# Performance work log

Measured on AMD Instinct MI355X. Metric: run time of the kernel, lower is better.

Reference implementation:

```python
import jax, jax.numpy as jnp
import numpy as np

NUM_HEADS = 24
HEAD_DIM = 128
EPS = 1e-6


def setup_inputs() -> dict:
    key = jax.random.key(0)
    k0, k1, k2 = jax.random.split(key, 3)
    B, S, dim = 2, 2048, 3072
    hidden_states = jax.random.normal(k0, (B, S, dim), dtype=jnp.float32)
    image_rotary_emb = jax.random.normal(k1, (1, 1, S, HEAD_DIM // 2, 2, 2), dtype=jnp.float32)
    w_qkv = jax.random.normal(k2, (dim, 3 * dim), dtype=jnp.float32) * 0.02
    b_qkv = jnp.zeros((3 * dim,), dtype=jnp.float32)
    norm_q_w = jnp.ones((HEAD_DIM,), dtype=jnp.float32)
    norm_k_w = jnp.ones((HEAD_DIM,), dtype=jnp.float32)
    return {
        "hidden_states": hidden_states,
        "image_rotary_emb": image_rotary_emb,
        "w_qkv": w_qkv,
        "b_qkv": b_qkv,
        "norm_q_w": norm_q_w,
        "norm_k_w": norm_k_w,
    }


def _rmsnorm(x, w):
    # RMSNorm over last dim (head_dim)
    var = jnp.mean(x * x, axis=-1, keepdims=True)
    return x * jax.lax.rsqrt(var + EPS) * w


def _apply_rope(x, freqs_cis):
    # x: [B,H,S,D]; freqs_cis: [1,1,S,D//2,2,2]
    B, H, S, D = x.shape
    x_ = x.reshape(B, H, S, D // 2, 1, 2)
    out = freqs_cis[..., 0] * x_[..., 0] + freqs_cis[..., 1] * x_[..., 1]  # [B,H,S,D//2,2]
    return out.reshape(B, H, S, D)


def reference(hidden_states, image_rotary_emb, w_qkv, b_qkv, norm_q_w, norm_k_w):
    B, S, _ = hidden_states.shape
    H, D = NUM_HEADS, HEAD_DIM
    qkv = hidden_states @ w_qkv + b_qkv                 # [B,S,3*H*D]
    qkv = qkv.reshape(B, S, 3, H, D)
    q = jnp.moveaxis(qkv[:, :, 0], 1, 2)                # [B,H,S,D]
    k = jnp.moveaxis(qkv[:, :, 1], 1, 2)
    v = jnp.moveaxis(qkv[:, :, 2], 1, 2)
    q = _rmsnorm(q, norm_q_w)
    k = _rmsnorm(k, norm_k_w)
    q = _apply_rope(q, image_rotary_emb)
    k = _apply_rope(k, image_rotary_emb)
    scale = 1.0 / jnp.sqrt(jnp.asarray(D, dtype=q.dtype))
    scores = jnp.einsum("bhqd,bhkd->bhqk", q, k) * scale
    attn = jax.nn.softmax(scores, axis=-1)
    out = jnp.einsum("bhqk,bhkd->bhqd", attn, v)        # [B,H,S,D]
    out = jnp.moveaxis(out, 1, 2).reshape(B, S, H * D)  # [B,S,H*D]
    return out
```

## Files before the change

### kernel.cpp

```cpp
#include <hip/hip_runtime.h>


#define SS 2048
#define BB 2
#define HH 24
#define DD 128
#define KDIM 3072
#define N3 9216
#define MM 4096

typedef float f32x4 __attribute__((ext_vector_type(4)));
typedef __bf16 bf16x8 __attribute__((ext_vector_type(8)));

__device__ __forceinline__ unsigned short f2b(float f) {
  union { float f; unsigned int u; } v; v.f = f;
  unsigned int u = v.u;
  u += 0x7FFFu + ((u >> 16) & 1u);
  return (unsigned short)(u >> 16);
}
__device__ __forceinline__ float b2f(unsigned short b) {
  union { unsigned int u; float f; } v; v.u = ((unsigned int)b) << 16; return v.f;
}
__device__ __forceinline__ f32x4 mfma16(bf16x8 a, bf16x8 b, f32x4 c) {
  return __builtin_amdgcn_mfma_f32_16x16x32_bf16(a, b, c, 0, 0, 0);
}
typedef __attribute__((address_space(1))) void gas_void;
typedef __attribute__((address_space(3))) void las_void;
__device__ __forceinline__ void load_lds16(const void* g, void* l) {
  __builtin_amdgcn_global_load_lds((gas_void*)g, (las_void*)l, 16, 0, 0);
}
__device__ __forceinline__ int swz(int row, int byteInRow) {
  return byteInRow ^ ((row & 7) << 4);
}

__global__ void cvt_bf16(const float* __restrict__ in, unsigned short* __restrict__ out, int n4) {
  int i = blockIdx.x * 256 + threadIdx.x;
  if (i >= n4) return;
  float4 v = reinterpret_cast<const float4*>(in)[i];
  ushort4 o;
  o.x = f2b(v.x); o.y = f2b(v.y); o.z = f2b(v.z); o.w = f2b(v.w);
  reinterpret_cast<ushort4*>(out)[i] = o;
}

__global__ void transpose_w(const float* __restrict__ w, unsigned short* __restrict__ wt) {
  __shared__ float tile[32][33];
  int n0 = blockIdx.x * 32, k0 = blockIdx.y * 32;
  int tx = threadIdx.x, ty = threadIdx.y;
#pragma unroll
  for (int i = 0; i < 4; i++)
    tile[ty + 8 * i][tx] = w[(size_t)(k0 + ty + 8 * i) * N3 + n0 + tx];
  __syncthreads();
#pragma unroll
  for (int i = 0; i < 4; i++)
    wt[(size_t)(n0 + ty + 8 * i) * KDIM + k0 + tx] = f2b(tile[tx][ty + 8 * i]);
}

__global__ __launch_bounds__(256, 2) void gemm_qkv(
    const unsigned short* __restrict__ A, const unsigned short* __restrict__ Bt,
    const float* __restrict__ bias, unsigned short* __restrict__ qkv) {
  __shared__ __align__(16) unsigned short As[128 * 64];
  __shared__ __align__(16) unsigned short Bs[128 * 64];
  const int tid = threadIdx.x;
  const int wave = tid >> 6, lane = tid & 63;
  const int wm = wave >> 1, wn = wave & 1;
  const int g = lane >> 4, lr = lane & 15;
  const int m0 = blockIdx.x * 128, n0 = blockIdx.y * 128;

  f32x4 acc[4][4] = {};

  for (int k0 = 0; k0 < KDIM; k0 += 64) {
    __syncthreads();
#pragma unroll
    for (int i = 0; i < 4; i++) {
      int c = wave * 4 + i;
      int row = c * 8 + (lane >> 3);
      int kk = (lane & 7) * 8;
      load_lds16(A + (size_t)(m0 + row) * KDIM + k0 + kk, &As[c * 512]);
      load_lds16(Bt + (size_t)(n0 + row) * KDIM + k0 + kk, &Bs[c * 512]);
    }
    __syncthreads();
#pragma unroll
    for (int kk = 0; kk < 64; kk += 32) {
      bf16x8 af[4], bfr[4];
#pragma unroll
      for (int i = 0; i < 4; i++) {
        af[i]  = *reinterpret_cast<const bf16x8*>(&As[(wm * 64 + i * 16 + lr) * 64 + kk + g * 8]);
        bfr[i] = *reinterpret_cast<const bf16x8*>(&Bs[(wn * 64 + i * 16 + lr) * 64 + kk + g * 8]);
      }
#pragma unroll
      for (int i = 0; i < 4; i++)
#pragma unroll
        for (int j = 0; j < 4; j++)
          acc[i][j] = mfma16(af[i], bfr[j], acc[i][j]);
    }
  }

  const int which = n0 / 3072;
  const int h = (n0 % 3072) / 128;
#pragma unroll
  for (int bj = 0; bj < 4; bj++) {
    int d = wn * 64 + bj * 16 + lr;
    float bv = bias[n0 + d];
#pragma unroll
    for (int ai = 0; ai < 4; ai++) {
#pragma unroll
      for (int r = 0; r < 4; r++) {
        int m = m0 + wm * 64 + ai * 16 + g * 4 + r;
        int b = m >> 11, s = m & 2047;
        float val = acc[ai][bj][r] + bv;
        qkv[((((size_t)which * BB + b) * HH + h) * SS + s) * DD + d] = f2b(val);
      }
    }
  }
}

__global__ void rms_rope(unsigned short* qkv, const float* __restrict__ freqs,
                         const float* __restrict__ wq, const float* __restrict__ wk) {
  int row = blockIdx.x * 4 + (threadIdx.x >> 6);
  int lane = threadIdx.x & 63;
  int s = row & 2047;
  int t = row >> 11;
  int which = t / (BB * HH);
  unsigned short* x = qkv + (size_t)row * DD;
  ushort2 xx = *reinterpret_cast<ushort2*>(&x[lane * 2]);
  float x0 = b2f(xx.x), x1 = b2f(xx.y);
  float ssum = x0 * x0 + x1 * x1;
#pragma unroll
  for (int off = 1; off < 64; off <<= 1) ssum += __shfl_xor(ssum, off);
  float rn = rsqrtf(ssum * (1.0f / 128.0f) + 1e-6f);
  const float* wgt = which ? wk : wq;
  x0 *= rn * wgt[lane * 2];
  x1 *= rn * wgt[lane * 2 + 1];
  float4 f = reinterpret_cast<const float4*>(freqs)[s * 64 + lane];
  ushort2 yy;
  yy.x = f2b(f.x * x0 + f.y * x1);
  yy.y = f2b(f.z * x0 + f.w * x1);
  *reinterpret_cast<ushort2*>(&x[lane * 2]) = yy;
}

__global__ void transpose_v(const unsigned short* __restrict__ qkv, unsigned short* __restrict__ vt) {
  __shared__ unsigned short tile[32][33];
  int bh = blockIdx.z;
  int s0 = blockIdx.x * 32, d0 = blockIdx.y * 32;
  const unsigned short* v = qkv + ((size_t)2 * BB * HH + bh) * SS * DD;
  int tx = threadIdx.x, ty = threadIdx.y;
#pragma unroll
  for (int i = 0; i < 4; i++)
    tile[ty + 8 * i][tx] = v[(size_t)(s0 + ty + 8 * i) * DD + d0 + tx];
  __syncthreads();
  unsigned short* o = vt + (size_t)bh * DD * SS;
#pragma unroll
  for (int i = 0; i < 4; i++)
    o[(size_t)(d0 + ty + 8 * i) * SS + s0 + tx] = tile[tx][ty + 8 * i];
}

__global__ __launch_bounds__(256, 2) void attn(
    const unsigned short* __restrict__ qkv, const unsigned short* __restrict__ vt,
    float* __restrict__ out) {
  __shared__ __align__(16) unsigned short Ks[64 * 128];
  __shared__ __align__(16) unsigned short Vs[128 * 64];
  __shared__ __align__(16) unsigned short Ps[4][16 * 64];
  const int bh = blockIdx.y;
  const int q0 = blockIdx.x * 64;
  const int wave = threadIdx.x >> 6, lane = threadIdx.x & 63;
  const int g = lane >> 4, lr = lane & 15;
  const unsigned short* Q   = qkv + (size_t)bh * SS * DD;
  const unsigned short* Kp  = qkv + ((size_t)BB * HH + bh) * SS * DD;
  const unsigned short* Vtp = vt + (size_t)bh * DD * SS;

  bf16x8 qf[4];
  {
    int qr = q0 + wave * 16 + lr;
#pragma unroll
    for (int kd = 0; kd < 4; kd++)
      qf[kd] = *reinterpret_cast<const bf16x8*>(&Q[(size_t)qr * DD + kd * 32 + g * 8]);
  }
  float mrow[4], lrow[4];
  f32x4 o[8] = {};
#pragma unroll
  for (int r = 0; r < 4; r++) { mrow[r] = -1e30f; lrow[r] = 0.f; }
  const float scale = 0.08838834764831845f;

  for (int kt = 0; kt < SS / 64; kt++) {
    int k0 = kt * 64;
    __syncthreads();
#pragma unroll
    for (int i = 0; i < 4; i++) {
      int c = wave * 4 + i;
      {
        int row = c * 4 + g;
        int lb = swz(row, lr * 16);
        load_lds16(Kp + (size_t)(k0 + row) * DD + (lb >> 1), &Ks[c * 512]);
      }
      {
        int row = c * 8 + (lane >> 3);
        int lb = swz(row, (lane & 7) * 16);
        load_lds16(Vtp + (size_t)row * SS + k0 + (lb >> 1), &Vs[c * 512]);
      }
    }
    __syncthreads();

    f32x4 sc[4] = {};
#pragma unroll
    for (int cf = 0; cf < 4; cf++) {
#pragma unroll
      for (int kd = 0; kd < 4; kd++) {
        int row = cf * 16 + lr;
        bf16x8 kb = *reinterpret_cast<const bf16x8*>(
            &Ks[(row * 256 + swz(row, kd * 64 + g * 16)) >> 1]);
        sc[cf] = mfma16(qf[kd], kb, sc[cf]);
      }
    }
#pragma unroll
    for (int cf = 0; cf < 4; cf++) sc[cf] *= scale;

#pragma unroll
    for (int r = 0; r < 4; r++) {
      float pm = fmaxf(fmaxf(sc[0][r], sc[1][r]), fmaxf(sc[2][r], sc[3][r]));
      pm = fmaxf(pm, __shfl_xor(pm, 1));
      pm = fmaxf(pm, __shfl_xor(pm, 2));
      pm = fmaxf(pm, __shfl_xor(pm, 4));
      pm = fmaxf(pm, __shfl_xor(pm, 8));
      float mnew = fmaxf(mrow[r], pm);
      float corr = __expf(mrow[r] - mnew);
      float psum = 0.f;
      int prow = g * 4 + r;
#pragma unroll
      for (int cf = 0; cf < 4; cf++) {
        float p = __expf(sc[cf][r] - mnew);
        psum += p;
        int col = cf * 16 + lr;
        Ps[wave][(prow * 128 + swz(prow, col * 2)) >> 1] = f2b(p);
      }
      psum += __shfl_xor(psum, 1);
      psum += __shfl_xor(psum, 2);
      psum += __shfl_xor(psum, 4);
      psum += __shfl_xor(psum, 8);
      lrow[r] = lrow[r] * corr + psum;
      mrow[r] = mnew;
#pragma unroll
      for (int dn = 0; dn < 8; dn++) o[dn][r] *= corr;
    }

#pragma unroll
    for (int ks = 0; ks < 2; ks++) {
      bf16x8 pa = *reinterpret_cast<const bf16x8*>(
          &Ps[wave][(lr * 128 + swz(lr, ks * 64 + g * 16)) >> 1]);
#pragma unroll
      for (int dn = 0; dn < 8; dn++) {
        int vrow = dn * 16 + lr;
        bf16x8 vb = *reinterpret_cast<const bf16x8*>(
            &Vs[(vrow * 128 + swz(vrow, ks * 64 + g * 16)) >> 1]);
        o[dn] = mfma16(pa, vb, o[dn]);
      }
    }
  }

  const int b = bh / HH, h = bh % HH;
#pragma unroll
  for (int r = 0; r < 4; r++) {
    int s = q0 + wave * 16 + g * 4 + r;
    float inv = 1.0f / lrow[r];
#pragma unroll
    for (int dn = 0; dn < 8; dn++) {
      int d = dn * 16 + lr;
      out[((size_t)b * SS + s) * 3072 + h * DD + d] = o[dn][r] * inv;
    }
  }
}

extern "C" void kernel_launch(void* const* d_in, const int* in_sizes, int n_in,
                              void* d_out, int out_size, void* d_ws, size_t ws_size,
                              hipStream_t stream) {
  const float* hs     = (const float*)d_in[0];
  const float* freqs  = (const float*)d_in[1];
  const float* w_qkv  = (const float*)d_in[2];
  const float* b_qkv  = (const float*)d_in[3];
  const float* norm_q = (const float*)d_in[4];
  const float* norm_k = (const float*)d_in[5];
  float* out = (float*)d_out;

  char* ws = (char*)d_ws;
  unsigned short* A_bf = (unsigned short*)(ws);
  unsigned short* Wt   = (unsigned short*)(ws + 25165824);
  unsigned short* qkv  = (unsigned short*)(ws + 81788928);
  unsigned short* Vt   = (unsigned short*)(ws + 157286400);

  cvt_bf16<<<dim3(12288), dim3(256), 0, stream>>>(hs, A_bf, 3145728);
  transpose_w<<<dim3(288, 96), dim3(32, 8), 0, stream>>>(w_qkv, Wt);
  gemm_qkv<<<dim3(32, 72), dim3(256), 0, stream>>>(A_bf, Wt, b_qkv, qkv);
  rms_rope<<<dim3(49152), dim3(256), 0, stream>>>(qkv, freqs, norm_q, norm_k);
  transpose_v<<<dim3(64, 4, 48), dim3(32, 8), 0, stream>>>(qkv, Vt);
  attn<<<dim3(32, 48), dim3(256), 0, stream>>>(qkv, Vt, out);
}
```

Baseline: 736.2 us.

## Rewrite QKV GEMM with 256x256 tiles, double-buffered LDS and block swizzle

```diff
diff --git a/kernel.cpp b/kernel.cpp
--- a/kernel.cpp
+++ b/kernel.cpp
@@ -8,6 +8,7 @@
 #define KDIM 3072
 #define N3 9216
 #define MM 4096
+#define NT 96
 
 typedef float f32x4 __attribute__((ext_vector_type(4)));
 typedef __bf16 bf16x8 __attribute__((ext_vector_type(8)));
@@ -55,60 +56,85 @@
     wt[(size_t)(n0 + ty + 8 * i) * KDIM + k0 + tx] = f2b(tile[tx][ty + 8 * i]);
 }
 
-__global__ __launch_bounds__(256, 2) void gemm_qkv(
+__global__ __launch_bounds__(512, 2) void gemm_qkv(
     const unsigned short* __restrict__ A, const unsigned short* __restrict__ Bt,
     const float* __restrict__ bias, unsigned short* __restrict__ qkv) {
-  __shared__ __align__(16) unsigned short As[128 * 64];
-  __shared__ __align__(16) unsigned short Bs[128 * 64];
+  __shared__ __align__(16) unsigned short As[2][8192];
+  __shared__ __align__(16) unsigned short Bs[2][8192];
   const int tid = threadIdx.x;
   const int wave = tid >> 6, lane = tid & 63;
-  const int wm = wave >> 1, wn = wave & 1;
+  const int wm = wave >> 2, wn = wave & 3;
   const int g = lane >> 4, lr = lane & 15;
-  const int m0 = blockIdx.x * 128, n0 = blockIdx.y * 128;
-
-  f32x4 acc[4][4] = {};
-
-  for (int k0 = 0; k0 < KDIM; k0 += 64) {
-    __syncthreads();
-#pragma unroll
-    for (int i = 0; i < 4; i++) {
-      int c = wave * 4 + i;
-      int row = c * 8 + (lane >> 3);
-      int kk = (lane & 7) * 8;
-      load_lds16(A + (size_t)(m0 + row) * KDIM + k0 + kk, &As[c * 512]);
-      load_lds16(Bt + (size_t)(n0 + row) * KDIM + k0 + kk, &Bs[c * 512]);
-    }
-    __syncthreads();
-#pragma unroll
-    for (int kk = 0; kk < 64; kk += 32) {
-      bf16x8 af[4], bfr[4];
-#pragma unroll
-      for (int i = 0; i < 4; i++) {
-        af[i]  = *reinterpret_cast<const bf16x8*>(&As[(wm * 64 + i * 16 + lr) * 64 + kk + g * 8]);
-        bfr[i] = *reinterpret_cast<const bf16x8*>(&Bs[(wn * 64 + i * 16 + lr) * 64 + kk + g * 8]);
-      }
-#pragma unroll
-      for (int i = 0; i < 4; i++)
-#pragma unroll
-        for (int j = 0; j < 4; j++)
-          acc[i][j] = mfma16(af[i], bfr[j], acc[i][j]);
-    }
-  }
-
-  const int which = n0 / 3072;
-  const int h = (n0 % 3072) / 128;
-#pragma unroll
-  for (int bj = 0; bj < 4; bj++) {
-    int d = wn * 64 + bj * 16 + lr;
-    float bv = bias[n0 + d];
-#pragma unroll
-    for (int ai = 0; ai < 4; ai++) {
+  const int swzid = (blockIdx.x & 7) * 72 + (blockIdx.x >> 3);
+  const int m0 = (swzid & 15) * 256, n0 = (swzid >> 4) * 256;
+  const unsigned short* Ag = A + (size_t)m0 * KDIM;
+  const unsigned short* Bg = Bt + (size_t)n0 * KDIM;
+
+  f32x4 acc[8][4] = {};
+  const int srow = lane >> 2;
+  const int sks = (lane & 3) * 8;
+
+#pragma unroll
+  for (int cc = 0; cc < 2; cc++) {
+    int c = wave * 2 + cc;
+    int m = c * 16 + srow;
+    load_lds16(Ag + (size_t)m * KDIM + sks, &As[0][c * 512]);
+    load_lds16(Bg + (size_t)m * KDIM + sks, &Bs[0][c * 512]);
+  }
+
+#define GTILE(K0, CUR, DOST, NK0, NXT, VM)                                     \
+  {                                                                            \
+    __builtin_amdgcn_s_barrier();                                              \
+    __builtin_amdgcn_sched_barrier(0);                                         \
+    if (DOST) {                                                                \
+      _Pragma("unroll") for (int cc = 0; cc < 2; cc++) {                       \
+        int c = wave * 2 + cc;                                                 \
+        int m = c * 16 + srow;                                                 \
+        load_lds16(Ag + (size_t)m * KDIM + (NK0) + sks, &As[NXT][c * 512]);    \
+        load_lds16(Bg + (size_t)m * KDIM + (NK0) + sks, &Bs[NXT][c * 512]);    \
+      }                                                                        \
+    }                                                                          \
+    asm volatile("s_waitcnt vmcnt(" #VM ")" ::: "memory");                     \
+    __builtin_amdgcn_sched_barrier(0);                                         \
+    bf16x8 af[8], bfr[4];                                                      \
+    _Pragma("unroll") for (int i = 0; i < 8; i++)                              \
+      af[i] = *reinterpret_cast<const bf16x8*>(                                \
+          &As[CUR][(wm * 128 + i * 16 + lr) * 32 + g * 8]);                    \
+    _Pragma("unroll") for (int j = 0; j < 4; j++)                              \
+      bfr[j] = *reinterpret_cast<const bf16x8*>(                               \
+          &Bs[CUR][(wn * 64 + j * 16 + lr) * 32 + g * 8]);                     \
+    __builtin_amdgcn_s_setprio(1);                                             \
+    _Pragma("unroll") for (int i = 0; i < 8; i++)                              \
+      _Pragma("unroll") for (int j = 0; j < 4; j++)                            \
+        acc[i][j] = mfma16(af[i], bfr[j], acc[i][j]);                          \
+    __builtin_amdgcn_s_setprio(0);                                             \
+  }
+
+  for (int t = 0; t < NT - 4; t += 2) {
+    GTILE(t * 32, 0, 1, (t + 1) * 32, 1, 4);
+    GTILE((t + 1) * 32, 1, 1, (t + 2) * 32, 0, 4);
+  }
+  GTILE((NT - 4) * 32, 0, 1, (NT - 3) * 32, 1, 4);
+  GTILE((NT - 3) * 32, 1, 1, (NT - 2) * 32, 0, 4);
+  GTILE((NT - 2) * 32, 0, 1, (NT - 1) * 32, 1, 4);
+  GTILE((NT - 1) * 32, 1, 0, 0, 0, 0);
+#undef GTILE
+
+#pragma unroll
+  for (int j = 0; j < 4; j++) {
+    int ng = n0 + wn * 64 + j * 16 + lr;
+    int which = ng / 3072;
+    int rem = ng - which * 3072;
+    int h = rem >> 7, d = rem & 127;
+    float bv = bias[ng];
+#pragma unroll
+    for (int i = 0; i < 8; i++) {
 #pragma unroll
       for (int r = 0; r < 4; r++) {
-        int m = m0 + wm * 64 + ai * 16 + g * 4 + r;
+        int m = m0 + wm * 128 + i * 16 + g * 4 + r;
         int b = m >> 11, s = m & 2047;
-        float val = acc[ai][bj][r] + bv;
-        qkv[((((size_t)which * BB + b) * HH + h) * SS + s) * DD + d] = f2b(val);
+        qkv[((((size_t)which * BB + b) * HH + h) * SS + s) * DD + d] =
+            f2b(acc[i][j][r] + bv);
       }
     }
   }
@@ -288,7 +314,7 @@
 
   cvt_bf16<<<dim3(12288), dim3(256), 0, stream>>>(hs, A_bf, 3145728);
   transpose_w<<<dim3(288, 96), dim3(32, 8), 0, stream>>>(w_qkv, Wt);
-  gemm_qkv<<<dim3(32, 72), dim3(256), 0, stream>>>(A_bf, Wt, b_qkv, qkv);
+  gemm_qkv<<<dim3(576), dim3(512), 0, stream>>>(A_bf, Wt, b_qkv, qkv);
   rms_rope<<<dim3(49152), dim3(256), 0, stream>>>(qkv, freqs, norm_q, norm_k);
   transpose_v<<<dim3(64, 4, 48), dim3(32, 8), 0, stream>>>(qkv, Vt);
   attn<<<dim3(32, 48), dim3(256), 0, stream>>>(qkv, Vt, out);
```

Result: slower. 839.4 us (+14.0%).

## Double-buffer K/V tiles in attention and skip softmax rescale lazily

Applied to the files above, without the earlier changes.

```diff
diff --git a/kernel.cpp b/kernel.cpp
--- a/kernel.cpp
+++ b/kernel.cpp
@@ -157,8 +157,8 @@
 __global__ __launch_bounds__(256, 2) void attn(
     const unsigned short* __restrict__ qkv, const unsigned short* __restrict__ vt,
     float* __restrict__ out) {
-  __shared__ __align__(16) unsigned short Ks[64 * 128];
-  __shared__ __align__(16) unsigned short Vs[128 * 64];
+  __shared__ __align__(16) unsigned short Ks[2][64 * 128];
+  __shared__ __align__(16) unsigned short Vs[2][128 * 64];
   __shared__ __align__(16) unsigned short Ps[4][16 * 64];
   const int bh = blockIdx.y;
   const int q0 = blockIdx.x * 64;
@@ -181,24 +181,28 @@
   for (int r = 0; r < 4; r++) { mrow[r] = -1e30f; lrow[r] = 0.f; }
   const float scale = 0.08838834764831845f;
 
-  for (int kt = 0; kt < SS / 64; kt++) {
-    int k0 = kt * 64;
-    __syncthreads();
-#pragma unroll
-    for (int i = 0; i < 4; i++) {
-      int c = wave * 4 + i;
-      {
-        int row = c * 4 + g;
-        int lb = swz(row, lr * 16);
-        load_lds16(Kp + (size_t)(k0 + row) * DD + (lb >> 1), &Ks[c * 512]);
-      }
-      {
-        int row = c * 8 + (lane >> 3);
-        int lb = swz(row, (lane & 7) * 16);
-        load_lds16(Vtp + (size_t)row * SS + k0 + (lb >> 1), &Vs[c * 512]);
-      }
-    }
-    __syncthreads();
+#define KV_STAGE(bb, k0v)                                                      \
+  _Pragma("unroll") for (int i = 0; i < 4; i++) {                              \
+    int c = wave * 4 + i;                                                      \
+    {                                             \
+      int row = c * 4 + g;                                                     \
+      int lb = swz(row, lr * 16);                                              \
+      load_lds16(Kp + (size_t)((k0v) + row) * DD + (lb >> 1), &Ks[bb][c * 512]); \
+    }                                                                          \
+    {                                             \
+      int row = c * 8 + (lane >> 3);                                           \
+      int lb = swz(row, (lane & 7) * 16);                                      \
+      load_lds16(Vtp + (size_t)row * SS + (k0v) + (lb >> 1), &Vs[bb][c * 512]); \
+    }                                                                          \
+  }
+
+  KV_STAGE(0, 0);
+  asm volatile("s_waitcnt vmcnt(0)" ::: "memory");
+  __builtin_amdgcn_s_barrier();
+
+  for (int kt = 0; kt < 32; kt++) {
+    const int cur = kt & 1;
+    if (kt < 31) { KV_STAGE(cur ^ 1, (kt + 1) * 64); }
 
     f32x4 sc[4] = {};
 #pragma unroll
@@ -207,13 +211,14 @@
       for (int kd = 0; kd < 4; kd++) {
         int row = cf * 16 + lr;
         bf16x8 kb = *reinterpret_cast<const bf16x8*>(
-            &Ks[(row * 256 + swz(row, kd * 64 + g * 16)) >> 1]);
+            &Ks[cur][(row * 256 + swz(row, kd * 64 + g * 16)) >> 1]);
         sc[cf] = mfma16(qf[kd], kb, sc[cf]);
       }
     }
 #pragma unroll
     for (int cf = 0; cf < 4; cf++) sc[cf] *= scale;
 
+    float pm4[4];
 #pragma unroll
     for (int r = 0; r < 4; r++) {
       float pm = fmaxf(fmaxf(sc[0][r], sc[1][r]), fmaxf(sc[2][r], sc[3][r]));
@@ -221,13 +226,29 @@
       pm = fmaxf(pm, __shfl_xor(pm, 2));
       pm = fmaxf(pm, __shfl_xor(pm, 4));
       pm = fmaxf(pm, __shfl_xor(pm, 8));
-      float mnew = fmaxf(mrow[r], pm);
-      float corr = __expf(mrow[r] - mnew);
+      pm4[r] = pm;
+    }
+    int need = 0;
+#pragma unroll
+    for (int r = 0; r < 4; r++) need |= (pm4[r] > mrow[r] + 8.0f) ? 1 : 0;
+    if (__any(need)) {
+#pragma unroll
+      for (int r = 0; r < 4; r++) {
+        float mnew = fmaxf(mrow[r], pm4[r]);
+        float corr = __expf(mrow[r] - mnew);
+        lrow[r] *= corr;
+#pragma unroll
+        for (int dn = 0; dn < 8; dn++) o[dn][r] *= corr;
+        mrow[r] = mnew;
+      }
+    }
+#pragma unroll
+    for (int r = 0; r < 4; r++) {
       float psum = 0.f;
       int prow = g * 4 + r;
 #pragma unroll
       for (int cf = 0; cf < 4; cf++) {
-        float p = __expf(sc[cf][r] - mnew);
+        float p = __expf(sc[cf][r] - mrow[r]);
         psum += p;
         int col = cf * 16 + lr;
         Ps[wave][(prow * 128 + swz(prow, col * 2)) >> 1] = f2b(p);
@@ -236,10 +257,7 @@
       psum += __shfl_xor(psum, 2);
       psum += __shfl_xor(psum, 4);
       psum += __shfl_xor(psum, 8);
-      lrow[r] = lrow[r] * corr + psum;
-      mrow[r] = mnew;
-#pragma unroll
-      for (int dn = 0; dn < 8; dn++) o[dn][r] *= corr;
+      lrow[r] += psum;
     }
 
 #pragma unroll
@@ -250,11 +268,15 @@
       for (int dn = 0; dn < 8; dn++) {
         int vrow = dn * 16 + lr;
         bf16x8 vb = *reinterpret_cast<const bf16x8*>(
-            &Vs[(vrow * 128 + swz(vrow, ks * 64 + g * 16)) >> 1]);
+            &Vs[cur][(vrow * 128 + swz(vrow, ks * 64 + g * 16)) >> 1]);
         o[dn] = mfma16(pa, vb, o[dn]);
       }
     }
-  }
+
+    asm volatile("s_waitcnt vmcnt(0)" ::: "memory");
+    __builtin_amdgcn_s_barrier();
+  }
+#undef KV_STAGE
 
   const int b = bh / HH, h = bh % HH;
 #pragma unroll
```

Measured after the change: 743.8 us. About the same (+1.0%).
